# Kernel optimization log

Hardware: AMD Instinct MI355X
Metric: run time of the kernel (lower is better)

Reference implementation:

```python
import jax, jax.numpy as jnp
import numpy as np

EPS = 1e-5  # torch LayerNorm default


def _score_branch(feat, g, b, W1, B1, W2, B2):
    # feat: [B, C, H, W] -> tokens [B, H*W, C]
    B, C, H, Wd = feat.shape
    tokens = jnp.transpose(feat, (0, 2, 3, 1)).reshape(B, H * Wd, C)
    mu = tokens.mean(-1, keepdims=True)
    var = jnp.mean(jnp.square(tokens - mu), axis=-1, keepdims=True)
    x = (tokens - mu) * jax.lax.rsqrt(var + EPS) * g + b
    h = jax.nn.gelu(jnp.einsum('btc,cd->btd', x, W1) + B1, approximate=False)
    s = jax.nn.sigmoid(jnp.einsum('btd,do->bto', h, W2) + B2)  # [B, HW, 1]
    return s.reshape(B, 1, H, Wd)


def setup_inputs() -> dict:
    key = jax.random.key(0)
    ks = jax.random.split(key, 6)
    M, B, C, H, W = 3, 16, 768, 48, 48
    Ch = C // 4
    return {
        'feat0': jax.random.normal(ks[0], (B, C, H, W), jnp.float32),
        'feat1': jax.random.normal(ks[1], (B, C, H, W), jnp.float32),
        'feat2': jax.random.normal(ks[2], (B, C, H, W), jnp.float32),
        'ln_g': jnp.ones((M, C), jnp.float32),
        'ln_b': jnp.zeros((M, C), jnp.float32),
        'w1': jax.random.normal(ks[3], (M, C, Ch), jnp.float32) * 0.02,
        'b1': jnp.zeros((M, Ch), jnp.float32),
        'w2': jax.random.normal(ks[4], (M, Ch, 1), jnp.float32) * 0.02,
        'b2': jnp.zeros((M, 1), jnp.float32),
    }


def reference(feat0, feat1, feat2, ln_g, ln_b, w1, b1, w2, b2):
    feats = (feat0, feat1, feat2)
    outs = []
    for i, feat in enumerate(feats):  # fixed small loop over modalities
        outs.append(_score_branch(feat, ln_g[i], ln_b[i], w1[i], b1[i], w2[i], b2[i]))
    return tuple(outs)
```

## Files before the change

kernel.cpp:

```cpp
#include <hip/hip_runtime.h>
#include <hip/hip_bf16.h>

typedef __attribute__((ext_vector_type(8))) short bf16x8;
typedef __attribute__((ext_vector_type(4))) short bf16x4;
typedef __attribute__((ext_vector_type(4))) float f32x4;

__device__ __forceinline__ unsigned short f2bf(float f) {
    __hip_bfloat16 h = __float2bfloat16(f);
    return __builtin_bit_cast(unsigned short, h);
}

#define BT 64
#define TPM 576
#define NCHUNK 24

__global__ void prep_partial(const float* __restrict__ w1, const float* __restrict__ lng,
                             const float* __restrict__ lnb,
                             float* __restrict__ upart, float* __restrict__ vpart)
{
    const int m   = blockIdx.x >> 3;
    const int seg = blockIdx.x & 7;
    const int d   = threadIdx.x;
    const float* w1m = w1 + (size_t)m * 768 * 192;
    const float* gm  = lng + m * 768;
    const float* bm  = lnb + m * 768;
    const int c0 = seg * 96;
    float su = 0.f, sv = 0.f;
    for (int c = 0; c < 96; ++c) {
        float wv = w1m[(size_t)(c0 + c) * 192 + d];
        su += gm[c0 + c] * wv;
        sv += bm[c0 + c] * wv;
    }
    upart[(m * 8 + seg) * 192 + d] = su;
    vpart[(m * 8 + seg) * 192 + d] = sv;
}

__global__ void prep_combine(const float* __restrict__ upart, const float* __restrict__ vpart,
                             const float* __restrict__ b1,
                             float* __restrict__ u, float* __restrict__ vb)
{
    const int m = blockIdx.x;
    const int d = threadIdx.x;
    float su = 0.f, sv = 0.f;
    for (int s = 0; s < 8; ++s) {
        su += upart[(m * 8 + s) * 192 + d];
        sv += vpart[(m * 8 + s) * 192 + d];
    }
    u[m * 192 + d]  = su;
    vb[m * 192 + d] = sv + b1[m * 192 + d];
}

__global__ void prep_pack(const float* __restrict__ w1, const float* __restrict__ lng,
                          unsigned short* __restrict__ w1f)
{
    const int m  = blockIdx.x / 24;
    const int kk = blockIdx.x % 24;
    const int tid = threadIdx.x;
    __shared__ float ws[32 * 192];
    const float* w1m = w1 + ((size_t)m * 768 + kk * 32) * 192;
    const float* gm  = lng + m * 768 + kk * 32;
    for (int i = tid; i < 6144; i += 256) {
        int cl = i / 192, d = i % 192;
        ws[i] = gm[cl] * w1m[(size_t)cl * 192 + d];
    }
    __syncthreads();
    unsigned short* outp = w1f + ((size_t)m * 24 + kk) * 6144;
    for (int i = tid; i < 6144; i += 256) {
        int nf   = i >> 9;
        int rem  = i & 511;
        int lane = rem >> 3;
        int j    = rem & 7;
        int cl   = ((lane >> 4) << 3) + j;
        int d    = (nf << 4) + (lane & 15);
        outp[i]  = f2bf(ws[cl * 192 + d]);
    }
}

__global__ __launch_bounds__(256, 3)
void fused_main(const float* __restrict__ f0, const float* __restrict__ f1,
                const float* __restrict__ f2,
                const unsigned short* __restrict__ w1f,
                const float* __restrict__ u_g, const float* __restrict__ vb_g,
                const float* __restrict__ w2_g, const float* __restrict__ b2_g,
                float* __restrict__ out)
{
    const int bx   = blockIdx.x;
    const int mod  = bx / TPM;
    const int tile = bx % TPM;
    const float* feat = (mod == 0) ? f0 : ((mod == 1) ? f1 : f2);
    const int T0   = tile * BT;
    const int bimg = T0 / 2304;
    const int hw0  = T0 % 2304;
    const float* fbase = feat + (size_t)bimg * 768 * 2304 + hw0;

    const int tid = threadIdx.x;
    const int l   = tid & 63;
    const int w   = tid >> 6;
    const int p   = l & 31;
    const int cg  = l >> 5;

    __shared__ unsigned short Atile[2][64][40];
    __shared__ float redS[4][64], redQ[4][64];
    __shared__ float mu_s[64], rs_s[64];
    __shared__ float red2[4][64];

    const unsigned short* w1fm = w1f + (size_t)mod * 24 * 6144;

    f32x4 acc[4][3];
    #pragma unroll
    for (int a = 0; a < 4; ++a)
        #pragma unroll
        for (int b = 0; b < 3; ++b) acc[a][b] = (f32x4){0.f, 0.f, 0.f, 0.f};

    float sum0 = 0.f, ssq0 = 0.f, sum1 = 0.f, ssq1 = 0.f;

    float2 avA[4], avB[4];
    bf16x8 bfA[3], bfB[3];

    auto LOADA = [&](float2 (&av)[4], int kk) {
        const float* sA = fbase + (size_t)(kk * 32 + w * 8 + cg * 4) * 2304 + 2 * p;
        #pragma unroll
        for (int j = 0; j < 4; ++j)
            av[j] = *reinterpret_cast<const float2*>(sA + (size_t)j * 2304);
    };
    auto LOADB = [&](bf16x8 (&bf)[3], int kk) {
        const bf16x8* sB = reinterpret_cast<const bf16x8*>(w1fm + (size_t)kk * 6144);
        #pragma unroll
        for (int nf = 0; nf < 3; ++nf)
            bf[nf] = sB[(w * 3 + nf) * 64 + l];
    };

    auto STEP = [&](float2 (&av)[4], bf16x8 (&bf)[3], int kk) {
        const int buf = kk & 1;
        const int t0 = 2 * p, t1 = t0 + 1;
        const int s0 = w ^ (((t0 >> 2) ^ (t0 >> 4)) & 3);
        const int s1 = w ^ (((t1 >> 2) ^ (t1 >> 4)) & 3);
        bf16x4 q0, q1;
        #pragma unroll
        for (int j = 0; j < 4; ++j) {
            float x0 = av[j].x, x1 = av[j].y;
            q0[j] = (short)f2bf(x0);
            q1[j] = (short)f2bf(x1);
            sum0 += x0; ssq0 += x0 * x0;
            sum1 += x1; ssq1 += x1 * x1;
        }
        *reinterpret_cast<bf16x4*>(&Atile[buf][t0][s0 * 8 + cg * 4]) = q0;
        *reinterpret_cast<bf16x4*>(&Atile[buf][t1][s1 * 8 + cg * 4]) = q1;
        int kn = kk + 2; if (kn > NCHUNK - 1) kn = NCHUNK - 1;
        LOADA(av, kn);
        asm volatile("s_waitcnt lgkmcnt(0)" ::: "memory");
        __builtin_amdgcn_sched_barrier(0);
        __builtin_amdgcn_s_barrier();
        const int col = l & 15, lg = l >> 4;
        #pragma unroll
        for (int mf = 0; mf < 4; ++mf) {
            int t = mf * 16 + col;
            int s = lg ^ (((t >> 2) ^ (t >> 4)) & 3);
            bf16x8 af = *reinterpret_cast<const bf16x8*>(&Atile[buf][t][s * 8]);
            #pragma unroll
            for (int nf = 0; nf < 3; ++nf)
                acc[mf][nf] = __builtin_amdgcn_mfma_f32_16x16x32_bf16(
                                  af, bf[nf], acc[mf][nf], 0, 0, 0);
        }
        LOADB(bf, kn);
    };

    LOADA(avA, 0); LOADB(bfA, 0);
    LOADA(avB, 1); LOADB(bfB, 1);
    #pragma unroll 1
    for (int kt = 0; kt < NCHUNK / 2; ++kt) {
        STEP(avA, bfA, 2 * kt);
        STEP(avB, bfB, 2 * kt + 1);
    }

    sum0 += __shfl_xor(sum0, 32);  sum1 += __shfl_xor(sum1, 32);
    ssq0 += __shfl_xor(ssq0, 32);  ssq1 += __shfl_xor(ssq1, 32);
    if (l < 32) {
        redS[w][2 * p] = sum0;  redS[w][2 * p + 1] = sum1;
        redQ[w][2 * p] = ssq0;  redQ[w][2 * p + 1] = ssq1;
    }
    __syncthreads();
    if (tid < 64) {
        float S = redS[0][tid] + redS[1][tid] + redS[2][tid] + redS[3][tid];
        float Q = redQ[0][tid] + redQ[1][tid] + redQ[2][tid] + redQ[3][tid];
        float mu = S * (1.f / 768.f);
        float var = Q * (1.f / 768.f) - mu * mu;
        mu_s[tid] = mu;
        rs_s[tid] = rsqrtf(var + 1e-5f);
    }
    __syncthreads();

    const int col = l & 15, lg = l >> 4;
    const float* um  = u_g  + mod * 192;
    const float* vbm = vb_g + mod * 192;
    const float* w2m = w2_g + mod * 192;
    float uf[3], vbf[3], w2f[3];
    #pragma unroll
    for (int nf = 0; nf < 3; ++nf) {
        int d = (w * 3 + nf) * 16 + col;
        uf[nf] = um[d]; vbf[nf] = vbm[d]; w2f[nf] = w2m[d];
    }
    float ps[4][4];
    #pragma unroll
    for (int mf = 0; mf < 4; ++mf) {
        #pragma unroll
        for (int r = 0; r < 4; ++r) {
            int t = mf * 16 + lg * 4 + r;
            float mu = mu_s[t], rs = rs_s[t];
            float pp = 0.f;
            #pragma unroll
            for (int nf = 0; nf < 3; ++nf) {
                float x = rs * (acc[mf][nf][r] - mu * uf[nf]) + vbf[nf];
                float h = 0.5f * x * (1.f + erff(x * 0.70710678118f));
                pp += h * w2f[nf];
            }
            ps[mf][r] = pp;
        }
    }
    #pragma unroll
    for (int m = 1; m < 16; m <<= 1)
        #pragma unroll
        for (int mf = 0; mf < 4; ++mf)
            #pragma unroll
            for (int r = 0; r < 4; ++r)
                ps[mf][r] += __shfl_xor(ps[mf][r], m, 64);
    if (col == 0) {
        #pragma unroll
        for (int mf = 0; mf < 4; ++mf)
            #pragma unroll
            for (int r = 0; r < 4; ++r)
                red2[w][mf * 16 + lg * 4 + r] = ps[mf][r];
    }
    __syncthreads();
    if (tid < 64) {
        float logit = red2[0][tid] + red2[1][tid] + red2[2][tid] + red2[3][tid] + b2_g[mod];
        out[(size_t)mod * 36864 + T0 + tid] = 1.f / (1.f + expf(-logit));
    }
}

extern "C" void kernel_launch(void* const* d_in, const int* in_sizes, int n_in,
                              void* d_out, int out_size, void* d_ws, size_t ws_size,
                              hipStream_t stream)
{
    const float* f0  = (const float*)d_in[0];
    const float* f1  = (const float*)d_in[1];
    const float* f2  = (const float*)d_in[2];
    const float* lng = (const float*)d_in[3];
    const float* lnb = (const float*)d_in[4];
    const float* w1  = (const float*)d_in[5];
    const float* b1  = (const float*)d_in[6];
    const float* w2  = (const float*)d_in[7];
    const float* b2  = (const float*)d_in[8];
    float* out = (float*)d_out;

    char* ws = (char*)d_ws;
    unsigned short* w1f = (unsigned short*)ws;
    float* u     = (float*)(ws + 884736);
    float* vb    = (float*)(ws + 887040);
    float* upart = (float*)(ws + 889344);
    float* vpart = (float*)(ws + 907776);

    prep_partial<<<dim3(24), dim3(192), 0, stream>>>(w1, lng, lnb, upart, vpart);
    prep_combine<<<dim3(3),  dim3(192), 0, stream>>>(upart, vpart, b1, u, vb);
    prep_pack   <<<dim3(72), dim3(256), 0, stream>>>(w1, lng, w1f);
    fused_main  <<<dim3(3 * TPM), dim3(256), 0, stream>>>(f0, f1, f2, w1f, u, vb, w2, b2, out);
}
```

Baseline: 106.1 us.

## Stage feature tiles via async global-to-LDS loads with four-deep pipeline

The register-based double-buffered activation loads are replaced with direct global_load_lds transfers into a four-stage LDS ring. Per-step vmcnt waits and barriers hand off data, and a single bf16 A tile is reused. The aim is to keep more HBM reads in flight and free registers. In exchange it adds LDS usage (32KB staging), which may lower occupancy, and the vmcnt accounting is fragile, since a miscount would consume stale data.

After: 122.4 us. 1.15x slower.

```diff
diff --git a/kernel.cpp b/kernel.cpp
--- a/kernel.cpp
+++ b/kernel.cpp
@@ -4,15 +4,25 @@
 typedef __attribute__((ext_vector_type(8))) short bf16x8;
 typedef __attribute__((ext_vector_type(4))) short bf16x4;
 typedef __attribute__((ext_vector_type(4))) float f32x4;
+typedef __attribute__((address_space(1))) const unsigned int gu32;
+typedef __attribute__((address_space(3))) unsigned int lu32;
 
 __device__ __forceinline__ unsigned short f2bf(float f) {
     __hip_bfloat16 h = __float2bfloat16(f);
     return __builtin_bit_cast(unsigned short, h);
 }
 
+template<int N> __device__ __forceinline__ void waitv() {
+    asm volatile("s_waitcnt vmcnt(%0)" :: "i"(N) : "memory");
+}
+__device__ __forceinline__ void waitlgkm0() {
+    asm volatile("s_waitcnt lgkmcnt(0)" ::: "memory");
+}
+
 #define BT 64
 #define TPM 576
 #define NCHUNK 24
+#define DEPTH 4
 
 __global__ void prep_partial(const float* __restrict__ w1, const float* __restrict__ lng,
                              const float* __restrict__ lnb,
@@ -98,8 +108,10 @@
     const int w   = tid >> 6;
     const int p   = l & 31;
     const int cg  = l >> 5;
-
-    __shared__ unsigned short Atile[2][64][40];
+    const int col = l & 15, lg = l >> 4;
+
+    __shared__ float Fstage[DEPTH][32][64];
+    __shared__ unsigned short Atile[64][40];
     __shared__ float redS[4][64], redQ[4][64];
     __shared__ float mu_s[64], rs_s[64];
     __shared__ float red2[4][64];
@@ -113,64 +125,78 @@
         for (int b = 0; b < 3; ++b) acc[a][b] = (f32x4){0.f, 0.f, 0.f, 0.f};
 
     float sum0 = 0.f, ssq0 = 0.f, sum1 = 0.f, ssq1 = 0.f;
-
-    float2 avA[4], avB[4];
-    bf16x8 bfA[3], bfB[3];
-
-    auto LOADA = [&](float2 (&av)[4], int kk) {
-        const float* sA = fbase + (size_t)(kk * 32 + w * 8 + cg * 4) * 2304 + 2 * p;
-        #pragma unroll
-        for (int j = 0; j < 4; ++j)
-            av[j] = *reinterpret_cast<const float2*>(sA + (size_t)j * 2304);
-    };
-    auto LOADB = [&](bf16x8 (&bf)[3], int kk) {
+    bf16x8 bf[3];
+
+    auto STAGE = [&](int src_kk, int qb) {
+        #pragma unroll
+        for (int j = 0; j < 2; ++j) {
+            const float* src = fbase + (size_t)(src_kk * 32 + w * 8 + j * 4 + lg) * 2304
+                                     + 4 * (l & 15);
+            __builtin_amdgcn_global_load_lds((gu32*)src,
+                                             (lu32*)&Fstage[qb][w * 8 + j * 4][0],
+                                             16, 0, 0);
+        }
+    };
+    auto LOADB = [&](int kk) {
         const bf16x8* sB = reinterpret_cast<const bf16x8*>(w1fm + (size_t)kk * 6144);
         #pragma unroll
         for (int nf = 0; nf < 3; ++nf)
             bf[nf] = sB[(w * 3 + nf) * 64 + l];
     };
-
-    auto STEP = [&](float2 (&av)[4], bf16x8 (&bf)[3], int kk) {
-        const int buf = kk & 1;
+    auto TOPB = [&]() {
+        __builtin_amdgcn_sched_barrier(0);
+        __builtin_amdgcn_s_barrier();
+        __builtin_amdgcn_sched_barrier(0);
+    };
+
+    auto STEPR = [&](int kk, int qb) {
         const int t0 = 2 * p, t1 = t0 + 1;
         const int s0 = w ^ (((t0 >> 2) ^ (t0 >> 4)) & 3);
         const int s1 = w ^ (((t1 >> 2) ^ (t1 >> 4)) & 3);
         bf16x4 q0, q1;
         #pragma unroll
         for (int j = 0; j < 4; ++j) {
-            float x0 = av[j].x, x1 = av[j].y;
-            q0[j] = (short)f2bf(x0);
-            q1[j] = (short)f2bf(x1);
-            sum0 += x0; ssq0 += x0 * x0;
-            sum1 += x1; ssq1 += x1 * x1;
-        }
-        *reinterpret_cast<bf16x4*>(&Atile[buf][t0][s0 * 8 + cg * 4]) = q0;
-        *reinterpret_cast<bf16x4*>(&Atile[buf][t1][s1 * 8 + cg * 4]) = q1;
-        int kn = kk + 2; if (kn > NCHUNK - 1) kn = NCHUNK - 1;
-        LOADA(av, kn);
-        asm volatile("s_waitcnt lgkmcnt(0)" ::: "memory");
+            float2 v = *reinterpret_cast<const float2*>(&Fstage[qb][w * 8 + cg * 4 + j][t0]);
+            q0[j] = (short)f2bf(v.x);
+            q1[j] = (short)f2bf(v.y);
+            sum0 += v.x; ssq0 += v.x * v.x;
+            sum1 += v.y; ssq1 += v.y * v.y;
+        }
+        *reinterpret_cast<bf16x4*>(&Atile[t0][s0 * 8 + cg * 4]) = q0;
+        *reinterpret_cast<bf16x4*>(&Atile[t1][s1 * 8 + cg * 4]) = q1;
+        waitlgkm0();
+        TOPB();
+        int kn = kk + DEPTH; if (kn > NCHUNK - 1) kn = NCHUNK - 1;
+        STAGE(kn, qb);
         __builtin_amdgcn_sched_barrier(0);
-        __builtin_amdgcn_s_barrier();
-        const int col = l & 15, lg = l >> 4;
+        bf16x8 af[4];
         #pragma unroll
         for (int mf = 0; mf < 4; ++mf) {
             int t = mf * 16 + col;
             int s = lg ^ (((t >> 2) ^ (t >> 4)) & 3);
-            bf16x8 af = *reinterpret_cast<const bf16x8*>(&Atile[buf][t][s * 8]);
+            af[mf] = *reinterpret_cast<const bf16x8*>(&Atile[t][s * 8]);
+        }
+        #pragma unroll
+        for (int mf = 0; mf < 4; ++mf)
             #pragma unroll
             for (int nf = 0; nf < 3; ++nf)
                 acc[mf][nf] = __builtin_amdgcn_mfma_f32_16x16x32_bf16(
-                                  af, bf[nf], acc[mf][nf], 0, 0, 0);
-        }
-        LOADB(bf, kn);
-    };
-
-    LOADA(avA, 0); LOADB(bfA, 0);
-    LOADA(avB, 1); LOADB(bfB, 1);
+                                  af[mf], bf[nf], acc[mf][nf], 0, 0, 0);
+        int kb = kk + 1; if (kb > NCHUNK - 1) kb = NCHUNK - 1;
+        LOADB(kb);
+    };
+
+    STAGE(0, 0); STAGE(1, 1); STAGE(2, 2); STAGE(3, 3);
+    __builtin_amdgcn_sched_barrier(0);
+    LOADB(0);
+    __builtin_amdgcn_sched_barrier(0);
+
+    waitv<9>();  TOPB(); STEPR(0, 0);
+    waitv<12>(); TOPB(); STEPR(1, 1);
+    waitv<15>(); TOPB(); STEPR(2, 2);
     #pragma unroll 1
-    for (int kt = 0; kt < NCHUNK / 2; ++kt) {
-        STEP(avA, bfA, 2 * kt);
-        STEP(avB, bfB, 2 * kt + 1);
+    for (int kk = 3; kk < NCHUNK; ++kk) {
+        waitv<18>(); TOPB(); STEPR(kk, kk & 3);
     }
 
     sum0 += __shfl_xor(sum0, 32);  sum1 += __shfl_xor(sum1, 32);
@@ -190,7 +216,6 @@
     }
     __syncthreads();
 
-    const int col = l & 15, lg = l >> 4;
     const float* um  = u_g  + mod * 192;
     const float* vbm = vb_g + mod * 192;
     const float* w2m = w2_g + mod * 192;
```
